# Kernel tuning notes

Measured on AMD Instinct MI355X. Metric: run time of the kernel, lower is better.

## Reference

```python
import jax, jax.numpy as jnp
import numpy as np

N = 50000
E = 800000
IN_CH = 128
OUT_CH = 32
HEADS = 2
NEG_SLOPE = 0.2


def setup_inputs() -> dict:
    key = jax.random.key(0)
    k_x, k_ei, k_w, k_as, k_ad, k_b = jax.random.split(key, 6)
    x = jax.random.normal(k_x, (N, IN_CH), dtype=jnp.float32)
    edge_index = jax.random.randint(k_ei, (2, E), 0, N, dtype=jnp.int64)
    # Glorot-style init scale for linear weight and attention vectors
    w_scale = 1.0 / np.sqrt(IN_CH)
    W = jax.random.normal(k_w, (IN_CH, HEADS * OUT_CH), dtype=jnp.float32) * w_scale
    a_scale = 1.0 / np.sqrt(OUT_CH)
    a_src = jax.random.normal(k_as, (HEADS, OUT_CH), dtype=jnp.float32) * a_scale
    a_dst = jax.random.normal(k_ad, (HEADS, OUT_CH), dtype=jnp.float32) * a_scale
    bias = jnp.zeros((HEADS * OUT_CH,), dtype=jnp.float32)
    return {"x": x, "edge_index": edge_index, "W": W, "a_src": a_src,
            "a_dst": a_dst, "bias": bias}


def reference(x, edge_index, W, a_src, a_dst, bias):
    n = x.shape[0]
    # add self-loops (add_self_loops=True); static shape E+N
    loops = jnp.tile(jnp.arange(n, dtype=edge_index.dtype), (2, 1))
    ei = jnp.concatenate([edge_index, loops], axis=1)
    src, dst = ei[0], ei[1]

    # linear projection -> per-head features [N, H, C]
    h = (x @ W).reshape(n, HEADS, OUT_CH)

    # per-node attention logits [N, H]
    alpha_s = jnp.sum(h * a_src[None], axis=-1)
    alpha_d = jnp.sum(h * a_dst[None], axis=-1)

    # per-edge score, LeakyReLU, segment softmax over edges grouped by dst
    e = jax.nn.leaky_relu(alpha_s[src] + alpha_d[dst], NEG_SLOPE)  # [E', H]
    e_max = jax.ops.segment_max(e, dst, num_segments=n)           # [N, H]
    e_exp = jnp.exp(e - e_max[dst])
    denom = jax.ops.segment_sum(e_exp, dst, num_segments=n)       # [N, H]
    alpha = e_exp / (denom[dst] + 1e-16)                          # [E', H]

    # scatter-add weighted messages [N, H, C]
    out = jax.ops.segment_sum(alpha[:, :, None] * h[src], dst, num_segments=n)
    # concat heads + bias (concat=True)
    return out.reshape(n, HEADS * OUT_CH) + bias
```

## Files before the change

### kernel.cpp

```cpp
#include <hip/hip_runtime.h>
#include <hip/hip_bf16.h>
#include <hip/hip_fp16.h>
#include <math.h>

#define IN_CH   128
#define OUT_CH  32
#define HEADS   2
#define HC      (HEADS * OUT_CH)
#define NEG_SLOPE 0.2f

#define NODE_TILE 64

#define HIST_ILP 2

#define BIN_CAP 64

typedef _Float16 h2_t __attribute__((ext_vector_type(2)));
union V16 { int4 v; h2_t h[4]; };

__device__ __forceinline__ float fdot2(h2_t a, h2_t b, float c) {
#if __has_builtin(__builtin_amdgcn_fdot2)
    return __builtin_amdgcn_fdot2(a, b, c, false);
#else
    return c + (float)a.x * (float)b.x + (float)a.y * (float)b.y;
#endif
}

__global__ __launch_bounds__(256) void gemm_hist_kernel(
    const float* __restrict__ x, const float* __restrict__ W,
    const float* __restrict__ a_src, const float* __restrict__ a_dst,
    __half* __restrict__ h, float* __restrict__ alpha_s, float* __restrict__ alpha_d,
    const int* __restrict__ src, const int* __restrict__ dst,
    int* __restrict__ deg, int* __restrict__ bins4,
    int n_nodes, int n_edges, int n_total, int gemm_blocks)
{
    const int tid = threadIdx.x;

    if (blockIdx.x >= gemm_blocks) {
        const int base = (blockIdx.x - gemm_blocks) * (256 * HIST_ILP) + tid;
        int d[HIST_ILP], s[HIST_ILP];
        #pragma unroll
        for (int i = 0; i < HIST_ILP; ++i) {
            int e = base + i * 256;
            if (e < n_total) {
                if (e < n_edges) { s[i] = src[e]; d[i] = dst[e]; }
                else             { s[i] = d[i] = e - n_edges; }
            }
        }
        int rk[HIST_ILP];
        #pragma unroll
        for (int i = 0; i < HIST_ILP; ++i) {
            int e = base + i * 256;
            if (e < n_total) rk[i] = atomicAdd(&deg[d[i]], 1);
        }
        #pragma unroll
        for (int i = 0; i < HIST_ILP; ++i) {
            int e = base + i * 256;
            if (e < n_total && rk[i] < BIN_CAP)
                bins4[(size_t)d[i] * BIN_CAP + rk[i]] = s[i];
        }
        return;
    }

    __shared__ _Float16 Wt[HC * IN_CH];
    __shared__ _Float16 Xs[NODE_TILE * IN_CH];

    const int node0 = blockIdx.x * NODE_TILE;

    const float4* W4 = (const float4*)W;
    #pragma unroll
    for (int i = 0; i < 8; ++i) {
        int idx4 = tid + i * 256;
        int k  = idx4 >> 4;
        int c4 = idx4 & 15;
        float4 v = W4[idx4];
        int chunk = k >> 3, klo = k & 7;
        _Float16 vals[4] = {(_Float16)v.x, (_Float16)v.y, (_Float16)v.z, (_Float16)v.w};
        #pragma unroll
        for (int r = 0; r < 4; ++r) {
            int col = c4 * 4 + r;
            int gc  = (col >> 3) & 7;
            Wt[col * IN_CH + ((chunk ^ gc) << 3) + klo] = vals[r];
        }
    }

    const float4* X4 = (const float4*)x;
    #pragma unroll
    for (int i = 0; i < 8; ++i) {
        int idx4 = tid + i * 256;
        int r = idx4 >> 5, c4 = idx4 & 31;
        int node = node0 + r;
        float4 v = make_float4(0.f, 0.f, 0.f, 0.f);
        if (node < n_nodes) v = X4[(size_t)node * (IN_CH / 4) + c4];
        _Float16 hv[4] = {(_Float16)v.x, (_Float16)v.y, (_Float16)v.z, (_Float16)v.w};
        int ofs = r * IN_CH + (((c4 >> 1) ^ (r & 7)) << 3) + (c4 & 1) * 4;
        *(int2*)&Xs[ofs] = *(int2*)hv;
    }
    __syncthreads();

    const int n    = tid >> 3;
    const int g    = tid & 7;
    const int col0 = g * 8;
    const int head = col0 >> 5;
    const int c0   = col0 & 31;

    float accA[8] = {0,0,0,0,0,0,0,0};
    float accB[8] = {0,0,0,0,0,0,0,0};
    const _Float16* xa = &Xs[n * IN_CH];
    const _Float16* xb = &Xs[(n + 32) * IN_CH];
    const int xkey = n & 7;

    for (int k0 = 0; k0 < IN_CH; k0 += 8) {
        const int chunk = k0 >> 3;
        const int xofs  = ((chunk ^ xkey) << 3);
        V16 va, vb;
        va.v = *(const int4*)&xa[xofs];
        vb.v = *(const int4*)&xb[xofs];
        const _Float16* wbase = &Wt[col0 * IN_CH + ((chunk ^ g) << 3)];
        #pragma unroll
        for (int j = 0; j < 8; ++j) {
            V16 w;
            w.v = *(const int4*)&wbase[j * IN_CH];
            float a = accA[j], b = accB[j];
            a = fdot2(w.h[0], va.h[0], a); b = fdot2(w.h[0], vb.h[0], b);
            a = fdot2(w.h[1], va.h[1], a); b = fdot2(w.h[1], vb.h[1], b);
            a = fdot2(w.h[2], va.h[2], a); b = fdot2(w.h[2], vb.h[2], b);
            a = fdot2(w.h[3], va.h[3], a); b = fdot2(w.h[3], vb.h[3], b);
            accA[j] = a; accB[j] = b;
        }
    }

    float asr[8], adr[8];
    #pragma unroll
    for (int j = 0; j < 8; ++j) {
        asr[j] = a_src[head * OUT_CH + c0 + j];
        adr[j] = a_dst[head * OUT_CH + c0 + j];
    }

    #pragma unroll
    for (int half = 0; half < 2; ++half) {
        const float* acc = half ? accB : accA;
        const int node = node0 + n + half * 32;
        if (node < n_nodes) {
            unsigned u[8];
            #pragma unroll
            for (int j = 0; j < 8; ++j) u[j] = __half_as_ushort(__float2half_rn(acc[j]));
            int4 v = make_int4((int)(u[0] | (u[1] << 16)), (int)(u[2] | (u[3] << 16)),
                               (int)(u[4] | (u[5] << 16)), (int)(u[6] | (u[7] << 16)));
            *(int4*)&h[(size_t)node * HC + col0] = v;
        }
        float ps = 0.f, pd = 0.f;
        #pragma unroll
        for (int j = 0; j < 8; ++j) { ps += acc[j] * asr[j]; pd += acc[j] * adr[j]; }
        ps += __shfl_xor(ps, 1); ps += __shfl_xor(ps, 2);
        pd += __shfl_xor(pd, 1); pd += __shfl_xor(pd, 2);
        if ((g & 3) == 0 && node < n_nodes) {
            alpha_s[node * HEADS + head] = ps;
            alpha_d[node * HEADS + head] = pd;
        }
    }
}

__global__ __launch_bounds__(256) void node_gather_kernel(
    const int* __restrict__ bins4, const int* __restrict__ deg,
    const float* __restrict__ alpha_s, const float* __restrict__ alpha_d,
    const __half* __restrict__ h, const float* __restrict__ bias,
    float* __restrict__ out, int n_nodes)
{
    __shared__ int2 stage[4][BIN_CAP];
    const int w = threadIdx.x >> 6;
    int node = blockIdx.x * 4 + w;
    if (node >= n_nodes) return;
    const int lane = threadIdx.x & 63;
    int cnt = deg[node];
    if (cnt > BIN_CAP) cnt = BIN_CAP;

    float2 adn = ((const float2*)alpha_d)[node];

    int sreg = 0;
    float p0 = 0.f, p1 = 0.f;
    if (lane < cnt) {
        sreg = bins4[(size_t)node * BIN_CAP + lane];
        float2 a2 = ((const float2*)alpha_s)[sreg];
        float v0 = a2.x + adn.x;
        float v1 = a2.y + adn.y;
        v0 = (v0 > 0.f) ? v0 : NEG_SLOPE * v0;
        v1 = (v1 > 0.f) ? v1 : NEG_SLOPE * v1;
        p0 = __expf(v0);
        p1 = __expf(v1);
    }

    unsigned u0 = __half_as_ushort(__float2half_rn(p0));
    unsigned u1 = __half_as_ushort(__float2half_rn(p1));
    float q0 = __half2float(__ushort_as_half((unsigned short)u0));
    float q1 = __half2float(__ushort_as_half((unsigned short)u1));

    #pragma unroll
    for (int off = 1; off < 64; off <<= 1) {
        q0 += __shfl_xor(q0, off);
        q1 += __shfl_xor(q1, off);
    }

    stage[w][lane] = make_int2(sreg, (int)((u1 << 16) | u0));

    const int q = lane >> 4;
    const int c = lane & 15;
    const unsigned hshift = (unsigned)(c >> 3) << 4;
    const unsigned laneofs = (unsigned)c << 3;
    const char* hb = (const char*)h;

    float a0 = 0.f, a1 = 0.f, a2v = 0.f, a3 = 0.f;
    for (int i = 0; i < cnt; i += 8) {
        #pragma unroll
        for (int j = 0; j < 2; ++j) {
            int2 rec = stage[w][i + 4 * j + q];
            unsigned ofs = ((unsigned)rec.x << 7) + laneofs;
            int2 hv = *(const int2*)(hb + ofs);
            __half2 hlo = *(__half2*)&hv.x;
            __half2 hhi = *(__half2*)&hv.y;
            float pj = __half2float(__ushort_as_half(
                           (unsigned short)(((unsigned)rec.y) >> hshift)));
            float2 flo = __half22float2(hlo);
            float2 fhi = __half22float2(hhi);
            a0  += pj * flo.x;
            a1  += pj * flo.y;
            a2v += pj * fhi.x;
            a3  += pj * fhi.y;
        }
    }
    a0  += __shfl_xor(a0, 16);  a0  += __shfl_xor(a0, 32);
    a1  += __shfl_xor(a1, 16);  a1  += __shfl_xor(a1, 32);
    a2v += __shfl_xor(a2v, 16); a2v += __shfl_xor(a2v, 32);
    a3  += __shfl_xor(a3, 16);  a3  += __shfl_xor(a3, 32);

    if (lane < 16) {
        const float lsum = (c >> 3) ? q1 : q0;
        const float inv = 1.f / (lsum + 1e-16f);
        float4 b4 = ((const float4*)bias)[c];
        float4 o;
        o.x = a0  * inv + b4.x;
        o.y = a1  * inv + b4.y;
        o.z = a2v * inv + b4.z;
        o.w = a3  * inv + b4.w;
        ((float4*)out)[(size_t)node * (HC / 4) + c] = o;
    }
}

extern "C" void kernel_launch(void* const* d_in, const int* in_sizes, int n_in,
                              void* d_out, int out_size, void* d_ws, size_t ws_size,
                              hipStream_t stream)
{
    const float* x      = (const float*)d_in[0];
    const int*   ei     = (const int*)d_in[1];
    const float* W      = (const float*)d_in[2];
    const float* a_src  = (const float*)d_in[3];
    const float* a_dst  = (const float*)d_in[4];
    const float* bias   = (const float*)d_in[5];
    float* out = (float*)d_out;

    const int n_nodes = in_sizes[0] / IN_CH;
    const int n_edges = in_sizes[1] / 2;
    const int n_total = n_edges + n_nodes;

    const int* src = ei;
    const int* dst = ei + n_edges;

    __half* h      = (__half*)d_ws;
    float* alpha_s = (float*)(h + (size_t)n_nodes * HC);
    float* alpha_d = alpha_s + (size_t)n_nodes * HEADS;
    int* deg       = (int*)(alpha_d + (size_t)n_nodes * HEADS);
    int* bins4     = deg + n_nodes;

    const int hist_blocks = (n_total + 256 * HIST_ILP - 1) / (256 * HIST_ILP);
    const int gemm_blocks = (n_nodes + NODE_TILE - 1) / NODE_TILE;

    hipMemsetAsync(deg, 0, (size_t)n_nodes * sizeof(int), stream);

    gemm_hist_kernel<<<gemm_blocks + hist_blocks, 256, 0, stream>>>(
        x, W, a_src, a_dst, h, alpha_s, alpha_d,
        src, dst, deg, bins4, n_nodes, n_edges, n_total, gemm_blocks);

    int ng_blocks = (n_nodes + 3) / 4;
    node_gather_kernel<<<ng_blocks, 256, 0, stream>>>(
        bins4, deg, alpha_s, alpha_d, h, bias, out, n_nodes);
}
```

Baseline: 160.0 us.

## Split fused GEMM/histogram kernel into separate kernels and raise histogram ILP

Measured after the change: 163.1 us. No clear change (+1.9%).

```diff
diff --git a/kernel.cpp b/kernel.cpp
--- a/kernel.cpp
+++ b/kernel.cpp
@@ -11,7 +11,7 @@
 
 #define NODE_TILE 64
 
-#define HIST_ILP 2
+#define HIST_ILP 4
 
 #define BIN_CAP 64
 
@@ -26,41 +26,40 @@
 #endif
 }
 
-__global__ __launch_bounds__(256) void gemm_hist_kernel(
+__global__ __launch_bounds__(256) void hist_fill_kernel(
+    const int* __restrict__ src, const int* __restrict__ dst,
+    int* __restrict__ deg, int* __restrict__ bins4,
+    int n_edges, int n_total)
+{
+    const int base = blockIdx.x * (256 * HIST_ILP) + threadIdx.x;
+    int s[HIST_ILP], d[HIST_ILP];
+    bool v[HIST_ILP];
+    #pragma unroll
+    for (int i = 0; i < HIST_ILP; ++i) {
+        int e = base + i * 256;
+        v[i] = (e < n_total);
+        if (v[i]) {
+            if (e < n_edges) { s[i] = src[e]; d[i] = dst[e]; }
+            else             { s[i] = d[i] = e - n_edges; }
+        }
+    }
+    int rk[HIST_ILP];
+    #pragma unroll
+    for (int i = 0; i < HIST_ILP; ++i)
+        if (v[i]) rk[i] = atomicAdd(&deg[d[i]], 1);
+    #pragma unroll
+    for (int i = 0; i < HIST_ILP; ++i)
+        if (v[i] && rk[i] < BIN_CAP)
+            bins4[(size_t)d[i] * BIN_CAP + rk[i]] = s[i];
+}
+
+__global__ __launch_bounds__(256) void gemm_logits_kernel(
     const float* __restrict__ x, const float* __restrict__ W,
     const float* __restrict__ a_src, const float* __restrict__ a_dst,
     __half* __restrict__ h, float* __restrict__ alpha_s, float* __restrict__ alpha_d,
-    const int* __restrict__ src, const int* __restrict__ dst,
-    int* __restrict__ deg, int* __restrict__ bins4,
-    int n_nodes, int n_edges, int n_total, int gemm_blocks)
+    int n_nodes)
 {
     const int tid = threadIdx.x;
-
-    if (blockIdx.x >= gemm_blocks) {
-        const int base = (blockIdx.x - gemm_blocks) * (256 * HIST_ILP) + tid;
-        int d[HIST_ILP], s[HIST_ILP];
-        #pragma unroll
-        for (int i = 0; i < HIST_ILP; ++i) {
-            int e = base + i * 256;
-            if (e < n_total) {
-                if (e < n_edges) { s[i] = src[e]; d[i] = dst[e]; }
-                else             { s[i] = d[i] = e - n_edges; }
-            }
-        }
-        int rk[HIST_ILP];
-        #pragma unroll
-        for (int i = 0; i < HIST_ILP; ++i) {
-            int e = base + i * 256;
-            if (e < n_total) rk[i] = atomicAdd(&deg[d[i]], 1);
-        }
-        #pragma unroll
-        for (int i = 0; i < HIST_ILP; ++i) {
-            int e = base + i * 256;
-            if (e < n_total && rk[i] < BIN_CAP)
-                bins4[(size_t)d[i] * BIN_CAP + rk[i]] = s[i];
-        }
-        return;
-    }
 
     __shared__ _Float16 Wt[HC * IN_CH];
     __shared__ _Float16 Xs[NODE_TILE * IN_CH];
@@ -276,9 +275,11 @@
 
     hipMemsetAsync(deg, 0, (size_t)n_nodes * sizeof(int), stream);
 
-    gemm_hist_kernel<<<gemm_blocks + hist_blocks, 256, 0, stream>>>(
-        x, W, a_src, a_dst, h, alpha_s, alpha_d,
-        src, dst, deg, bins4, n_nodes, n_edges, n_total, gemm_blocks);
+    hist_fill_kernel<<<hist_blocks, 256, 0, stream>>>(
+        src, dst, deg, bins4, n_edges, n_total);
+
+    gemm_logits_kernel<<<gemm_blocks, 256, 0, stream>>>(
+        x, W, a_src, a_dst, h, alpha_s, alpha_d, n_nodes);
 
     int ng_blocks = (n_nodes + 3) / 4;
     node_gather_kernel<<<ng_blocks, 256, 0, stream>>>(
```
